# Optimization experiments

Hardware: AMD Instinct MI355X
Metric: run time of the kernel (lower is better)

The kernel has to match this reference:

```python
import jax, jax.numpy as jnp
import numpy as np

C = 768
HEADS = 12

def setup_inputs() -> dict:
    key = jax.random.key(0)
    k1, k2, k3 = jax.random.split(key, 3)
    x = jax.random.normal(k1, (8, C, 32, 32), dtype=jnp.float32)
    # 1x1 convs are channel-wise linear maps; store as [out_c, in_c]
    w_qkv = jax.random.normal(k2, (3 * C, C), dtype=jnp.float32) * (C ** -0.5)
    w_proj = jax.random.normal(k3, (C, C), dtype=jnp.float32) * (C ** -0.5)
    return {"x": x, "w_qkv": w_qkv, "w_proj": w_proj}

def reference(x, w_qkv, w_proj):
    b, c, h, w = x.shape
    heads = HEADS
    dh = c // heads
    n = h * w
    scale = dh ** -0.5
    # 1x1 conv QKV: [b, 3c, h, w] -> [b, 3, heads, dh, n]
    qkv = jnp.einsum('oc,bchw->bohw', w_qkv, x).reshape(b, 3, heads, dh, n)
    q, k, v = qkv[:, 0], qkv[:, 1], qkv[:, 2]  # each [b, heads, dh, n]
    attn = jnp.einsum('bhdn,bhdm->bhnm', q, k) * scale  # [b, heads, n, n]
    attn = jax.nn.softmax(attn, axis=-1)
    out = jnp.einsum('bhnm,bhdm->bhdn', attn, v)  # [b, heads, dh, n]
    out = out.reshape(b, c, h, w)
    return jnp.einsum('oc,bchw->bohw', w_proj, out)
```

## Files before the change

### kernel.cpp

```cpp
#include <hip/hip_runtime.h>

typedef unsigned short u16;
typedef unsigned int u32;
typedef float v4f __attribute__((ext_vector_type(4)));
typedef __bf16 bf16x8 __attribute__((ext_vector_type(8)));

#define BATCH 8
#define CDIM 768
#define NHEAD 12
#define DH 64
#define NSEQ 1024
#define SCL 0.18033688011112042f

__device__ __forceinline__ u16 f2bf(float f) {
  u32 u = __builtin_bit_cast(u32, f);
  u += 0x7fffu + ((u >> 16) & 1u);
  return (u16)(u >> 16);
}

__device__ __forceinline__ u16 b16(float f) {
  return (u16)((__builtin_bit_cast(u32, f) + 0x8000u) >> 16);
}

__device__ __forceinline__ u32 pkbf(float hi, float lo) {
  u32 a = __builtin_bit_cast(u32, hi) + 0x8000u;
  u32 b = __builtin_bit_cast(u32, lo) + 0x8000u;
  return __builtin_amdgcn_perm(a, b, 0x07060302u);
}

__device__ __forceinline__ v4f mfma16(bf16x8 a, bf16x8 b, v4f c) {
  return __builtin_amdgcn_mfma_f32_16x16x32_bf16(a, b, c, 0, 0, 0);
}

__device__ __forceinline__ void gload16(const u16* g, u16* l) {
  __builtin_amdgcn_global_load_lds(
      (const __attribute__((address_space(1))) void*)g,
      (__attribute__((address_space(3))) void*)l, 16, 0, 0);
}

#define BARQ asm volatile("s_barrier" ::: "memory")
#define LGKM0 asm volatile("s_waitcnt lgkmcnt(0)" ::: "memory")
#define VMC0 asm volatile("s_waitcnt vmcnt(0)" ::: "memory")
#define FEN asm volatile("" ::: "memory")

__global__ __launch_bounds__(256) void k_prep(const float* __restrict__ x,
                                              const float* __restrict__ wq,
                                              const float* __restrict__ wp,
                                              u16* __restrict__ xT,
                                              u16* __restrict__ wqb,
                                              u16* __restrict__ wpb) {
  __shared__ u16 Ts[64][72];
  int bid = blockIdx.x;
  int t = threadIdx.x;
  if (bid < 2304) {
    bool isQ = bid < 1728;
    const float* s = isQ ? wq : wp;
    u16* d = isQ ? wqb : wpb;
    int i = (isQ ? bid : bid - 1728) * 256 + t;
    float4 v = ((const float4*)s)[i];
    u32 lo = (u32)f2bf(v.x) | ((u32)f2bf(v.y) << 16);
    u32 hi = (u32)f2bf(v.z) | ((u32)f2bf(v.w) << 16);
    ((uint2*)d)[i] = uint2{lo, hi};
    return;
  }
  int id = bid - 2304;
  int p0 = (id & 15) * 64; id >>= 4;
  int c0 = (id % 12) * 64; int b = id / 12;
  int cr = t >> 4;
  int p4 = (t & 15) * 4;
  const float* src = x + ((size_t)b * CDIM + c0) * NSEQ + p0;
#pragma unroll
  for (int i = 0; i < 4; ++i) {
    int c = cr + i * 16;
    float4 v = *(const float4*)&src[(size_t)c * NSEQ + p4];
    Ts[p4 + 0][c] = f2bf(v.x);
    Ts[p4 + 1][c] = f2bf(v.y);
    Ts[p4 + 2][c] = f2bf(v.z);
    Ts[p4 + 3][c] = f2bf(v.w);
  }
  __syncthreads();
  int p = t >> 2;
  int cq = t & 3;
  u16* dst = xT + ((size_t)b * NSEQ + p0 + p) * CDIM + c0;
#pragma unroll
  for (int j = 0; j < 2; ++j) {
    int ch = cq + j * 4;
    *(int4*)&dst[ch * 8] = *(const int4*)&Ts[p][ch * 8];
  }
}

#define NKT 24

__global__ __launch_bounds__(512, 2) void k_gemm_qkv(const u16* __restrict__ Wb,
                                                     const u16* __restrict__ xT,
                                                     u16* __restrict__ qkT,
                                                     u16* __restrict__ vbuf) {
  __shared__ u16 sm[3 * 17408];
  int bid = blockIdx.x;
  int swz = (bid & 7) * 32 + (bid >> 3);
  int oIdx = swz % 8, pIdx = swz / 8;
  int oT = oIdx * 288;
  int pG = pIdx * 256;

  int t = threadIdx.x, lane = t & 63, wid = t >> 6;
  int ln = lane & 15, quad = lane >> 4;
  int wm = wid >> 2, wn = wid & 3;

  int lrow = lane >> 2;
  int scg = ((lane & 3) ^ ((lane >> 3) & 3)) * 8;
  bool roleA = wid < 6;
  int w6 = wid - 6;
  const u16* Asrc = Wb + (size_t)(oT + wid * 48 + lrow) * CDIM + scg;
  const u16* Bsrc = xT + (size_t)(pG + (w6 < 0 ? 0 : w6) * 128 + lrow) * CDIM + scg;
  int ldA = wid * 1536;
  int ldB = 9216 + (w6 < 0 ? 0 : w6) * 4096;

#define STAGEQ(bi, kt) do {                                                \
    u16* bb_ = sm + (bi) * 17408;                                          \
    if (roleA) {                                                           \
      const u16* gp_ = Asrc + (kt) * 32;                                   \
      gload16(gp_, bb_ + ldA);                                             \
      gload16(gp_ + (size_t)16 * CDIM, bb_ + ldA + 512);                   \
      gload16(gp_ + (size_t)32 * CDIM, bb_ + ldA + 1024);                  \
    } else {                                                               \
      const u16* gp_ = Bsrc + (kt) * 32;                                   \
      _Pragma("unroll") for (int i_ = 0; i_ < 8; ++i_)                     \
        gload16(gp_ + (size_t)i_ * 16 * CDIM, bb_ + ldB + i_ * 512);       \
    }                                                                      \
  } while (0)

#define DRAINQ do {                                                        \
    if (roleA) asm volatile("s_waitcnt vmcnt(3)" ::: "memory");            \
    else asm volatile("s_waitcnt vmcnt(8)" ::: "memory");                  \
  } while (0)

  int slot = (quad ^ ((ln >> 1) & 3)) * 8;
  int rAr = (wm * 144 + ln) * 32;
  int rBr = 9216 + (wn * 64 + ln) * 32;

  v4f acc[9][4] = {};

  STAGEQ(0, 0);
  FEN;
  STAGEQ(1, 1);
  DRAINQ;
  BARQ;

  for (int j = 0; j < NKT; ++j) {
    const u16* sb = sm + (j % 3) * 17408;
    int bi2 = (j + 2) % 3;

    if (j < NKT - 2) STAGEQ(bi2, j + 2);
    bf16x8 af[5], bfr[4];
#pragma unroll
    for (int m = 0; m < 5; ++m)
      af[m] = *(const bf16x8*)&sb[rAr + m * 512 + slot];
#pragma unroll
    for (int n = 0; n < 4; ++n)
      bfr[n] = *(const bf16x8*)&sb[rBr + n * 512 + slot];
    BARQ;
    LGKM0;
    __builtin_amdgcn_sched_barrier(0);
    __builtin_amdgcn_s_setprio(1);
#pragma unroll
    for (int m = 0; m < 5; ++m)
#pragma unroll
      for (int n = 0; n < 4; ++n)
        acc[m][n] = mfma16(af[m], bfr[n], acc[m][n]);
    __builtin_amdgcn_s_setprio(0);
    BARQ;

    bf16x8 ag[4];
#pragma unroll
    for (int m = 0; m < 4; ++m)
      ag[m] = *(const bf16x8*)&sb[rAr + (m + 5) * 512 + slot];
    if (j < NKT - 2) DRAINQ;
    else if (j == NKT - 2) VMC0;
    BARQ;
    LGKM0;
    __builtin_amdgcn_sched_barrier(0);
    __builtin_amdgcn_s_setprio(1);
#pragma unroll
    for (int m = 0; m < 4; ++m)
#pragma unroll
      for (int n = 0; n < 4; ++n)
        acc[m + 5][n] = mfma16(ag[m], bfr[n], acc[m + 5][n]);
    __builtin_amdgcn_s_setprio(0);
    BARQ;
  }

#pragma unroll
  for (int m = 0; m < 9; ++m) {
#pragma unroll
    for (int n = 0; n < 4; ++n) {
      int ro = oT + wm * 144 + m * 16 + quad * 4;
      int cp = pG + wn * 64 + n * 16 + ln;
      int b = cp >> 10, p = cp & 1023;
      if (ro < 2 * CDIM) {
        u32 lo = (u32)f2bf(acc[m][n][0]) | ((u32)f2bf(acc[m][n][1]) << 16);
        u32 hi = (u32)f2bf(acc[m][n][2]) | ((u32)f2bf(acc[m][n][3]) << 16);
        *(uint2*)&qkT[((size_t)b * NSEQ + p) * 1536 + ro] = uint2{lo, hi};
      } else {
#pragma unroll
        for (int r = 0; r < 4; ++r)
          vbuf[((size_t)b * CDIM + (ro - 2 * CDIM + r)) * NSEQ + p] =
              f2bf(acc[m][n][r]);
      }
    }
  }
#undef STAGEQ
#undef DRAINQ
}

__global__ __launch_bounds__(256) void k_attn(const u16* __restrict__ qkT,
                                              const u16* __restrict__ vbuf,
                                              u16* __restrict__ attnT) {
  int id = blockIdx.x;
  int b = id & 7;
  int j = id >> 3;
  int h = j % 12;
  int nt0 = (j / 12) * 128;

  int t = threadIdx.x, lane = t & 63, wid = t >> 6;
  int ln = lane & 15, quad = lane >> 4;
  int nbase = nt0 + wid * 32;

  __shared__ u16 Ks[2][64 * 64];
  __shared__ u16 Vs[2][64 * 64];
  __shared__ u16 Pa[4][32 * 64];
  u16* myP = Pa[wid];

  const u16* qbase = qkT + ((size_t)b * NSEQ + nbase) * 1536 + h * DH;
  bf16x8 aq[2][2];
#pragma unroll
  for (int mt = 0; mt < 2; ++mt)
#pragma unroll
    for (int ks = 0; ks < 2; ++ks)
      aq[mt][ks] = *(const bf16x8*)&qbase[(size_t)(mt * 16 + ln) * 1536 + ks * 32 + quad * 8];

  bf16x8 ones;
#pragma unroll
  for (int i = 0; i < 8; ++i) ones[i] = __builtin_bit_cast(__bf16, (u16)0x3F80);

  v4f oacc[2][4] = {};
  v4f lacc[2] = {};

  int sr8 = lane >> 3;
  int sch = ((lane & 7) ^ sr8) * 8;
  const u16* kg0 = qkT + ((size_t)b * NSEQ + wid * 16 + sr8) * 1536 + CDIM + h * DH + sch;
  const u16* vg0 = vbuf + ((size_t)b * CDIM + h * DH + wid * 16 + sr8) * NSEQ + sch;
  int sK = wid * 1024;

  int sw0 = (quad ^ (ln & 7)) * 8;
  int sw1 = ((4 + quad) ^ (ln & 7)) * 8;
  int e7 = ln & 7;

#define STAGEK(kb, s_) do { size_t ko_ = (size_t)(s_) * 64 * 1536;          \
    gload16(kg0 + ko_, &Ks[kb][sK]);                                        \
    gload16(kg0 + ko_ + (size_t)8 * 1536, &Ks[kb][sK + 512]); } while (0)
#define STAGEV(vb, s_) do { int vo_ = (s_) * 64;                            \
    gload16(vg0 + vo_, &Vs[vb][sK]);                                        \
    gload16(vg0 + vo_ + 8 * NSEQ, &Vs[vb][sK + 512]); } while (0)

#define QKEXP(kb) do {                                                      \
    _Pragma("unroll") for (int ct = 0; ct < 4; ++ct) {                      \
      bf16x8 kf0 = *(const bf16x8*)&Ks[kb][(ct * 16 + ln) * 64 + sw0];      \
      bf16x8 kf1 = *(const bf16x8*)&Ks[kb][(ct * 16 + ln) * 64 + sw1];      \
      _Pragma("unroll") for (int mt = 0; mt < 2; ++mt) {                    \
        v4f sc = {};                                                        \
        sc = mfma16(kf0, aq[mt][0], sc);                                    \
        sc = mfma16(kf1, aq[mt][1], sc);                                    \
        float p0 = __builtin_amdgcn_exp2f(sc[0] * SCL);                     \
        float p1 = __builtin_amdgcn_exp2f(sc[1] * SCL);                     \
        float p2 = __builtin_amdgcn_exp2f(sc[2] * SCL);                     \
        float p3 = __builtin_amdgcn_exp2f(sc[3] * SCL);                     \
        int woff = (mt * 16 + ln) * 64 +                                    \
                   (((2 * ct + (quad >> 1)) ^ e7) * 8 + (quad & 1) * 4);    \
        *(uint2*)&myP[woff] = uint2{pkbf(p1, p0), pkbf(p3, p2)};            \
      }                                                                     \
    }                                                                       \
  } while (0)

#define READAP(ap) do {                                                     \
    _Pragma("unroll") for (int mt = 0; mt < 2; ++mt)                        \
      _Pragma("unroll") for (int ks = 0; ks < 2; ++ks)                      \
        ap[mt][ks] = *(const bf16x8*)&myP[(mt * 16 + ln) * 64 +             \
                                          ((ks * 4 + quad) ^ e7) * 8];      \
  } while (0)

#define PVSTEP(vb, ap) do {                                                 \
    __builtin_amdgcn_s_setprio(1);                                          \
    _Pragma("unroll") for (int mt = 0; mt < 2; ++mt) {                      \
      lacc[mt] = mfma16(ap[mt][0], ones, lacc[mt]);                         \
      lacc[mt] = mfma16(ap[mt][1], ones, lacc[mt]);                         \
    }                                                                       \
    __builtin_amdgcn_s_setprio(0);                                          \
    _Pragma("unroll") for (int nt = 0; nt < 4; ++nt) {                      \
      bf16x8 vf0 = *(const bf16x8*)&Vs[vb][(nt * 16 + ln) * 64 + sw0];      \
      bf16x8 vf1 = *(const bf16x8*)&Vs[vb][(nt * 16 + ln) * 64 + sw1];      \
      __builtin_amdgcn_s_setprio(1);                                        \
      _Pragma("unroll") for (int mt = 0; mt < 2; ++mt) {                    \
        oacc[mt][nt] = mfma16(ap[mt][0], vf0, oacc[mt][nt]);                \
        oacc[mt][nt] = mfma16(ap[mt][1], vf1, oacc[mt][nt]);                \
      }                                                                     \
      __builtin_amdgcn_s_setprio(0);                                        \
    }                                                                       \
  } while (0)

  bf16x8 apA[2][2], apB[2][2];

  STAGEK(0, 0);
  STAGEV(0, 0);
  __syncthreads();
  QKEXP(0);
  STAGEK(1, 1);
  READAP(apA);

#pragma unroll 1
  for (int s = 0; s < 16; s += 2) {
    __syncthreads();
    if (s < 14) STAGEK(0, s + 2);
    STAGEV(1, s + 1);
    QKEXP(1);
    PVSTEP(0, apA);
    READAP(apB);
    __syncthreads();
    if (s < 13) STAGEK(1, s + 3);
    if (s < 14) {
      STAGEV(0, s + 2);
      QKEXP(0);
    }
    PVSTEP(1, apB);
    if (s < 14) READAP(apA);
  }

#undef STAGEK
#undef STAGEV
#undef QKEXP
#undef READAP
#undef PVSTEP

#pragma unroll
  for (int mt = 0; mt < 2; ++mt) {
#pragma unroll
    for (int r = 0; r < 4; ++r) {
      float inv = 1.0f / lacc[mt][r];
      int n = nbase + mt * 16 + quad * 4 + r;
      u16* dst = attnT + ((size_t)b * NSEQ + n) * CDIM + h * DH;
#pragma unroll
      for (int nt = 0; nt < 4; ++nt)
        dst[nt * 16 + ln] = b16(oacc[mt][nt][r] * inv);
    }
  }
}

__global__ __launch_bounds__(256, 2) void k_gemm_proj(const u16* __restrict__ Wb,
                                                      const u16* __restrict__ aT,
                                                      float* __restrict__ out) {
  __shared__ u16 sm[3 * 10240];
  int bid = blockIdx.x;
  int swz = (bid & 7) * 32 + (bid >> 3);
  int oIdx = swz % 4, pIdx = swz / 4;
  int oT = oIdx * 192;
  int pG = pIdx * 128;

  int t = threadIdx.x, lane = t & 63, wid = t >> 6;
  int ln = lane & 15, quad = lane >> 4;
  int wm = wid >> 1, wn = wid & 1;

  int lrow = lane >> 2;
  int scg = ((lane & 3) ^ ((lane >> 3) & 3)) * 8;
  bool roleA = wid < 3;
  const u16* Asrc = Wb + (size_t)(oT + wid * 64 + lrow) * CDIM + scg;
  const u16* Bsrc = aT + (size_t)(pG + lrow) * CDIM + scg;
  int ldA = wid * 2048;
  int ldB = 6144;

#define STAGEP(bi, kt) do {                                                \
    u16* bb_ = sm + (bi) * 10240;                                          \
    if (roleA) {                                                           \
      const u16* gp_ = Asrc + (kt) * 32;                                   \
      _Pragma("unroll") for (int i_ = 0; i_ < 4; ++i_)                     \
        gload16(gp_ + (size_t)i_ * 16 * CDIM, bb_ + ldA + i_ * 512);       \
    } else {                                                               \
      const u16* gp_ = Bsrc + (kt) * 32;                                   \
      _Pragma("unroll") for (int i_ = 0; i_ < 8; ++i_)                     \
        gload16(gp_ + (size_t)i_ * 16 * CDIM, bb_ + ldB + i_ * 512);       \
    }                                                                      \
  } while (0)

#define DRAINP do {                                                        \
    if (roleA) asm volatile("s_waitcnt vmcnt(4)" ::: "memory");            \
    else asm volatile("s_waitcnt vmcnt(8)" ::: "memory");                  \
  } while (0)

  int slot = (quad ^ ((ln >> 1) & 3)) * 8;
  int rAr = (wm * 96 + ln) * 32;
  int rBr = 6144 + (wn * 64 + ln) * 32;

  v4f acc[6][4] = {};

  STAGEP(0, 0);
  FEN;
  STAGEP(1, 1);
  DRAINP;
  BARQ;

  for (int j = 0; j < NKT; ++j) {
    const u16* sb = sm + (j % 3) * 10240;
    int bi2 = (j + 2) % 3;

    if (j < NKT - 2) STAGEP(bi2, j + 2);
    bf16x8 af[3], bfr[4];
#pragma unroll
    for (int m = 0; m < 3; ++m)
      af[m] = *(const bf16x8*)&sb[rAr + m * 512 + slot];
#pragma unroll
    for (int n = 0; n < 4; ++n)
      bfr[n] = *(const bf16x8*)&sb[rBr + n * 512 + slot];
    BARQ;
    LGKM0;
    __builtin_amdgcn_sched_barrier(0);
    __builtin_amdgcn_s_setprio(1);
#pragma unroll
    for (int m = 0; m < 3; ++m)
#pragma unroll
      for (int n = 0; n < 4; ++n)
        acc[m][n] = mfma16(af[m], bfr[n], acc[m][n]);
    __builtin_amdgcn_s_setprio(0);
    BARQ;

    bf16x8 ag[3];
#pragma unroll
    for (int m = 0; m < 3; ++m)
      ag[m] = *(const bf16x8*)&sb[rAr + (m + 3) * 512 + slot];
    if (j < NKT - 2) DRAINP;
    else if (j == NKT - 2) VMC0;
    BARQ;
    LGKM0;
    __builtin_amdgcn_sched_barrier(0);
    __builtin_amdgcn_s_setprio(1);
#pragma unroll
    for (int m = 0; m < 3; ++m)
#pragma unroll
      for (int n = 0; n < 4; ++n)
        acc[m + 3][n] = mfma16(ag[m], bfr[n], acc[m + 3][n]);
    __builtin_amdgcn_s_setprio(0);
    BARQ;
  }

#pragma unroll
  for (int m = 0; m < 6; ++m) {
#pragma unroll
    for (int n = 0; n < 4; ++n) {
      int ro = oT + wm * 96 + m * 16 + quad * 4;
      int cp = pG + wn * 64 + n * 16 + ln;
      int b = cp >> 10, p = cp & 1023;
#pragma unroll
      for (int r = 0; r < 4; ++r)
        out[((size_t)b * CDIM + ro + r) * NSEQ + p] = acc[m][n][r];
    }
  }
#undef STAGEP
#undef DRAINP
}

extern "C" void kernel_launch(void* const* d_in, const int* in_sizes, int n_in,
                              void* d_out, int out_size, void* d_ws, size_t ws_size,
                              hipStream_t stream) {
  const float* x = (const float*)d_in[0];
  const float* w_qkv = (const float*)d_in[1];
  const float* w_proj = (const float*)d_in[2];
  float* out = (float*)d_out;

  char* ws = (char*)d_ws;
  u16* wqkv_bf = (u16*)(ws);
  u16* wproj_bf = (u16*)(ws + 3538944);
  u16* xT = (u16*)(ws + 4718592);
  u16* vbuf = (u16*)(ws + 17301504);
  u16* qkT = (u16*)d_out;
  u16* attnT = xT;

  k_prep<<<dim3(3840), dim3(256), 0, stream>>>(x, w_qkv, w_proj, xT, wqkv_bf, wproj_bf);
  k_gemm_qkv<<<dim3(256), dim3(512), 0, stream>>>(wqkv_bf, xT, qkT, vbuf);
  k_attn<<<dim3(768), dim3(256), 0, stream>>>(qkT, vbuf, attnT);
  k_gemm_proj<<<dim3(256), dim3(256), 0, stream>>>(wproj_bf, attnT, out);
}
```

Measured before the change: 172.4 us.

## Restructure QKV GEMM to double-buffered K=64 tiles with split staging

Replaces the QKV projection GEMM's triple-buffered K=32 pipeline with a double-buffered K=64 pipeline. That halves the number of outer iterations and the barrier and wait overhead per unit of work. Each next tile is loaded in two halves interleaved with the first two MFMA phases, with a new 8-way XOR swizzle for the wider rows. Shared memory rises from about 104KB to 139KB per block, which may limit the two blocks per CU requested by the launch bounds. The prefetch distance also shrinks from two stages to one.

```diff
diff --git a/kernel.cpp b/kernel.cpp
--- a/kernel.cpp
+++ b/kernel.cpp
@@ -89,13 +89,11 @@
   }
 }
 
-#define NKT 24
-
 __global__ __launch_bounds__(512, 2) void k_gemm_qkv(const u16* __restrict__ Wb,
                                                      const u16* __restrict__ xT,
                                                      u16* __restrict__ qkT,
                                                      u16* __restrict__ vbuf) {
-  __shared__ u16 sm[3 * 17408];
+  __shared__ u16 sm[2 * 34816];
   int bid = blockIdx.x;
   int swz = (bid & 7) * 32 + (bid >> 3);
   int oIdx = swz % 8, pIdx = swz / 8;
@@ -106,58 +104,53 @@
   int ln = lane & 15, quad = lane >> 4;
   int wm = wid >> 2, wn = wid & 3;
 
-  int lrow = lane >> 2;
-  int scg = ((lane & 3) ^ ((lane >> 3) & 3)) * 8;
+  int sr8 = lane >> 3;
+  int sch = ((lane & 7) ^ sr8) * 8;
   bool roleA = wid < 6;
   int w6 = wid - 6;
-  const u16* Asrc = Wb + (size_t)(oT + wid * 48 + lrow) * CDIM + scg;
-  const u16* Bsrc = xT + (size_t)(pG + (w6 < 0 ? 0 : w6) * 128 + lrow) * CDIM + scg;
-  int ldA = wid * 1536;
-  int ldB = 9216 + (w6 < 0 ? 0 : w6) * 4096;
-
-#define STAGEQ(bi, kt) do {                                                \
-    u16* bb_ = sm + (bi) * 17408;                                          \
+  const u16* Asrc = Wb + (size_t)(oT + wid * 48 + sr8) * CDIM + sch;
+  const u16* Bsrc = xT + (size_t)(pG + (w6 < 0 ? 0 : w6) * 128 + sr8) * CDIM + sch;
+  int ldA = wid * 3072;
+  int ldB = 18432 + (w6 < 0 ? 0 : w6) * 8192;
+
+#define STGH(bi, kt, h) do {                                               \
+    u16* bb_ = sm + (bi) * 34816;                                          \
     if (roleA) {                                                           \
-      const u16* gp_ = Asrc + (kt) * 32;                                   \
-      gload16(gp_, bb_ + ldA);                                             \
-      gload16(gp_ + (size_t)16 * CDIM, bb_ + ldA + 512);                   \
-      gload16(gp_ + (size_t)32 * CDIM, bb_ + ldA + 1024);                  \
+      const u16* gp_ = Asrc + (size_t)(kt) * 64;                           \
+      _Pragma("unroll") for (int i_ = 3 * (h); i_ < 3 * (h) + 3; ++i_)     \
+        gload16(gp_ + (size_t)i_ * 8 * CDIM, bb_ + ldA + i_ * 512);        \
     } else {                                                               \
-      const u16* gp_ = Bsrc + (kt) * 32;                                   \
-      _Pragma("unroll") for (int i_ = 0; i_ < 8; ++i_)                     \
-        gload16(gp_ + (size_t)i_ * 16 * CDIM, bb_ + ldB + i_ * 512);       \
+      const u16* gp_ = Bsrc + (size_t)(kt) * 64;                           \
+      _Pragma("unroll") for (int i_ = 8 * (h); i_ < 8 * (h) + 8; ++i_)     \
+        gload16(gp_ + (size_t)i_ * 8 * CDIM, bb_ + ldB + i_ * 512);        \
     }                                                                      \
   } while (0)
 
-#define DRAINQ do {                                                        \
-    if (roleA) asm volatile("s_waitcnt vmcnt(3)" ::: "memory");            \
-    else asm volatile("s_waitcnt vmcnt(8)" ::: "memory");                  \
-  } while (0)
-
-  int slot = (quad ^ ((ln >> 1) & 3)) * 8;
-  int rAr = (wm * 144 + ln) * 32;
-  int rBr = 9216 + (wn * 64 + ln) * 32;
+  int slot0 = (quad ^ (ln & 7)) * 8;
+  int slot1 = ((4 + quad) ^ (ln & 7)) * 8;
+  int rAr = (wm * 144 + ln) * 64;
+  int rBr = 18432 + (wn * 64 + ln) * 64;
 
   v4f acc[9][4] = {};
-
-  STAGEQ(0, 0);
-  FEN;
-  STAGEQ(1, 1);
-  DRAINQ;
+  bf16x8 af[5], bfr[4];
+
+  STGH(0, 0, 0);
+  STGH(0, 0, 1);
+  VMC0;
   BARQ;
 
-  for (int j = 0; j < NKT; ++j) {
-    const u16* sb = sm + (j % 3) * 17408;
-    int bi2 = (j + 2) % 3;
-
-    if (j < NKT - 2) STAGEQ(bi2, j + 2);
-    bf16x8 af[5], bfr[4];
+  for (int j = 0; j < 12; ++j) {
+    const u16* sb = sm + (j & 1) * 34816;
+    int nb = (j & 1) ^ 1;
+    bool nl = j < 11;
+
 #pragma unroll
     for (int m = 0; m < 5; ++m)
-      af[m] = *(const bf16x8*)&sb[rAr + m * 512 + slot];
+      af[m] = *(const bf16x8*)&sb[rAr + m * 1024 + slot0];
 #pragma unroll
     for (int n = 0; n < 4; ++n)
-      bfr[n] = *(const bf16x8*)&sb[rBr + n * 512 + slot];
+      bfr[n] = *(const bf16x8*)&sb[rBr + n * 1024 + slot0];
+    if (nl) STGH(nb, j + 1, 0);
     BARQ;
     LGKM0;
     __builtin_amdgcn_sched_barrier(0);
@@ -170,12 +163,10 @@
     __builtin_amdgcn_s_setprio(0);
     BARQ;
 
-    bf16x8 ag[4];
 #pragma unroll
     for (int m = 0; m < 4; ++m)
-      ag[m] = *(const bf16x8*)&sb[rAr + (m + 5) * 512 + slot];
-    if (j < NKT - 2) DRAINQ;
-    else if (j == NKT - 2) VMC0;
+      af[m] = *(const bf16x8*)&sb[rAr + (m + 5) * 1024 + slot0];
+    if (nl) STGH(nb, j + 1, 1);
     BARQ;
     LGKM0;
     __builtin_amdgcn_sched_barrier(0);
@@ -184,7 +175,41 @@
     for (int m = 0; m < 4; ++m)
 #pragma unroll
       for (int n = 0; n < 4; ++n)
-        acc[m + 5][n] = mfma16(ag[m], bfr[n], acc[m + 5][n]);
+        acc[m + 5][n] = mfma16(af[m], bfr[n], acc[m + 5][n]);
+    __builtin_amdgcn_s_setprio(0);
+    BARQ;
+
+#pragma unroll
+    for (int m = 0; m < 5; ++m)
+      af[m] = *(const bf16x8*)&sb[rAr + m * 1024 + slot1];
+#pragma unroll
+    for (int n = 0; n < 4; ++n)
+      bfr[n] = *(const bf16x8*)&sb[rBr + n * 1024 + slot1];
+    BARQ;
+    LGKM0;
+    __builtin_amdgcn_sched_barrier(0);
+    __builtin_amdgcn_s_setprio(1);
+#pragma unroll
+    for (int m = 0; m < 5; ++m)
+#pragma unroll
+      for (int n = 0; n < 4; ++n)
+        acc[m][n] = mfma16(af[m], bfr[n], acc[m][n]);
+    __builtin_amdgcn_s_setprio(0);
+    BARQ;
+
+#pragma unroll
+    for (int m = 0; m < 4; ++m)
+      af[m] = *(const bf16x8*)&sb[rAr + (m + 5) * 1024 + slot1];
+    if (nl) VMC0;
+    BARQ;
+    LGKM0;
+    __builtin_amdgcn_sched_barrier(0);
+    __builtin_amdgcn_s_setprio(1);
+#pragma unroll
+    for (int m = 0; m < 4; ++m)
+#pragma unroll
+      for (int n = 0; n < 4; ++n)
+        acc[m + 5][n] = mfma16(af[m], bfr[n], acc[m + 5][n]);
     __builtin_amdgcn_s_setprio(0);
     BARQ;
   }
@@ -208,8 +233,7 @@
       }
     }
   }
-#undef STAGEQ
-#undef DRAINQ
+#undef STGH
 }
 
 __global__ __launch_bounds__(256) void k_attn(const u16* __restrict__ qkT,
@@ -406,11 +430,11 @@
   DRAINP;
   BARQ;
 
-  for (int j = 0; j < NKT; ++j) {
+  for (int j = 0; j < 24; ++j) {
     const u16* sb = sm + (j % 3) * 10240;
     int bi2 = (j + 2) % 3;
 
-    if (j < NKT - 2) STAGEP(bi2, j + 2);
+    if (j < 22) STAGEP(bi2, j + 2);
     bf16x8 af[3], bfr[4];
 #pragma unroll
     for (int m = 0; m < 3; ++m)
@@ -434,8 +458,8 @@
 #pragma unroll
     for (int m = 0; m < 3; ++m)
       ag[m] = *(const bf16x8*)&sb[rAr + (m + 3) * 512 + slot];
-    if (j < NKT - 2) DRAINP;
-    else if (j == NKT - 2) VMC0;
+    if (j < 22) DRAINP;
+    else if (j == 22) VMC0;
     BARQ;
     LGKM0;
     __builtin_amdgcn_sched_barrier(0);
```

Result: no change. 171.4 us (-0.6%).
